# Optimization experiments

Hardware: AMD Instinct MI355X
Metric: run time of the kernel (lower is better)

The kernel has to match this reference:

```python
import jax, jax.numpy as jnp
import numpy as np

GROUPS = 32
EPS = 1e-5
NUM_HEADS = 8
HEAD_DIM = 64
CHANNELS = 512


def group_norm(x, scale, bias):
    # x: [b, h, w, c]; normalize over (h, w, channels-within-group)
    b, h, w, c = x.shape
    xg = x.reshape(b, h, w, GROUPS, c // GROUPS)
    mean = jnp.mean(xg, axis=(1, 2, 4), keepdims=True)
    var = jnp.var(xg, axis=(1, 2, 4), keepdims=True)
    xg = (xg - mean) * jax.lax.rsqrt(var + EPS)
    return xg.reshape(b, h, w, c) * scale + bias


def setup_inputs() -> dict:
    key = jax.random.key(0)
    ks = jax.random.split(key, 8)
    b, hs, ws, c = 8, 32, 32, CHANNELS
    inner = NUM_HEADS * HEAD_DIM
    return {
        "x": jax.random.normal(ks[0], (b, hs, ws, c), dtype=jnp.float32),
        "t": jax.random.normal(ks[1], (b,), dtype=jnp.float32),
        "gn_scale": jnp.ones((c,), dtype=jnp.float32),
        "gn_bias": jnp.zeros((c,), dtype=jnp.float32),
        "w_qkv": jax.random.normal(ks[2], (c, 3 * inner), dtype=jnp.float32) * 0.02,
        "b_qkv": jnp.zeros((3 * inner,), dtype=jnp.float32),
        "w_out": jax.random.normal(ks[3], (inner, c), dtype=jnp.float32) * 0.02,
        "b_out": jnp.zeros((c,), dtype=jnp.float32),
    }


def reference(x, t, gn_scale, gn_bias, w_qkv, b_qkv, w_out, b_out):
    b, hs, ws, c = x.shape
    # NOTE: original reassigns x = GroupNorm(x); the residual uses the NORMALIZED x.
    xn = group_norm(x, gn_scale, gn_bias)
    x_flat = xn.reshape(b, hs * ws, c)                      # [b, s, c]
    qkv = x_flat @ w_qkv + b_qkv                            # [b, s, 3*nh*hd]
    qkv = qkv.reshape(b, hs * ws, NUM_HEADS, 3 * HEAD_DIM)
    q, k, v = jnp.split(qkv, 3, axis=-1)                    # each [b, s, nh, hd]
    q = q / jnp.sqrt(jnp.float32(HEAD_DIM))
    q = q.transpose(0, 2, 1, 3)                             # [b, nh, s, hd]
    k = k.transpose(0, 2, 1, 3)
    v = v.transpose(0, 2, 1, 3)
    attn = jax.nn.softmax(jnp.einsum('bhqd,bhkd->bhqk', q, k), axis=-1)
    out = jnp.einsum('bhqk,bhkd->bhqd', attn, v)            # [b, nh, s, hd]
    out = out.transpose(0, 2, 1, 3).reshape(b, hs * ws, NUM_HEADS * HEAD_DIM)
    h = out @ w_out + b_out                                 # [b, s, c]
    h = h.reshape(b, hs, ws, c)
    return xn + h
```

## Files before the change

### kernel.cpp

```cpp
#include <hip/hip_runtime.h>
#include <hip/hip_bf16.h>


#define B_    8
#define S_    1024
#define C_    512
#define NH    8
#define HD    64
#define QKVC  1536
#define GROUPS 32
#define GSIZE  16
#define EPSV   1e-5f
#define QSCL  0.18033688f

using frag8 = __attribute__((ext_vector_type(8))) short;
using f32x4 = __attribute__((ext_vector_type(4))) float;

__device__ __forceinline__ float bf2f(unsigned short u) {
    union { unsigned int i; float f; } v; v.i = ((unsigned int)u) << 16; return v.f;
}
__device__ __forceinline__ unsigned short f2bf(float f) {
    union { float f; unsigned int i; } v; v.f = f;
    unsigned int x = v.i;
    return (unsigned short)((x + 0x7fffu + ((x >> 16) & 1u)) >> 16);
}
__device__ __forceinline__ unsigned int pk2bf(float a, float b) {
    union { float f; unsigned int u; } x, y; x.f = a; y.f = b;
    return __builtin_amdgcn_perm(y.u + 0x8000u, x.u + 0x8000u, 0x07060302u);
}
__device__ __forceinline__ float fexp2(float x) {
#if __has_builtin(__builtin_amdgcn_exp2f)
    return __builtin_amdgcn_exp2f(x);
#else
    return exp2f(x);
#endif
}
__device__ __forceinline__ f32x4 zero4() {
    f32x4 z; z[0] = 0.f; z[1] = 0.f; z[2] = 0.f; z[3] = 0.f; return z;
}
__device__ __forceinline__ void gl_lds(const unsigned short* gp, unsigned short* lp) {
    __builtin_amdgcn_global_load_lds(
        (const __attribute__((address_space(1))) void*)gp,
        (__attribute__((address_space(3))) void*)lp, 16, 0, 0);
}

__global__ __launch_bounds__(256) void prep_kernel(
        const float* __restrict__ w_qkv, const float* __restrict__ w_out,
        unsigned short* __restrict__ wqkvT, unsigned short* __restrict__ woutT,
        const float* __restrict__ x,
        const float* __restrict__ scale, const float* __restrict__ bias,
        unsigned short* __restrict__ xn) {
    __shared__ float tile[32][33];
    int id = blockIdx.x;
    int t = threadIdx.x;
    if (id < 1024) {
        const float* in; unsigned short* out; int N, n0, k0;
        if (id < 768) { in = w_qkv; out = wqkvT; N = QKVC; n0 = (id % 48) * 32; k0 = (id / 48) * 32; }
        else { int i2 = id - 768; in = w_out; out = woutT; N = C_; n0 = (i2 % 16) * 32; k0 = (i2 / 16) * 32; }
        for (int i = 0; i < 4; ++i) {
            int idx = t + i * 256; int r = idx >> 5, c = idx & 31;
            tile[r][c] = in[(size_t)(k0 + r) * N + n0 + c];
        }
        __syncthreads();
        for (int i = 0; i < 4; ++i) {
            int idx = t + i * 256; int r = idx >> 5, c = idx & 31;
            out[(size_t)(n0 + r) * C_ + k0 + c] = f2bf(tile[c][r]);
        }
        return;
    }
    int bg = id - 1024;
    int b = bg >> 5, g = bg & 31;
    const float* xb = x + (size_t)b * S_ * C_;

    float sum = 0.f, ss = 0.f;
    for (int i = 0; i < 16; ++i) {
        int idx = t + i * 256;
        int row = idx >> 2, j = idx & 3;
        float4 v = *(const float4*)(xb + (size_t)row * C_ + g * GSIZE + j * 4);
        sum += v.x + v.y + v.z + v.w;
        ss  += v.x * v.x + v.y * v.y + v.z * v.z + v.w * v.w;
    }
    for (int off = 1; off < 64; off <<= 1) {
        sum += __shfl_xor(sum, off);
        ss  += __shfl_xor(ss,  off);
    }
    __shared__ float s_sum[4], s_ss[4];
    int wid = t >> 6;
    if ((t & 63) == 0) { s_sum[wid] = sum; s_ss[wid] = ss; }
    __syncthreads();
    sum = s_sum[0] + s_sum[1] + s_sum[2] + s_sum[3];
    ss  = s_ss[0]  + s_ss[1]  + s_ss[2]  + s_ss[3];
    float mean = sum * (1.f / 16384.f);
    float var  = ss * (1.f / 16384.f) - mean * mean;
    float rinv = rsqrtf(var + EPSV);

    float sc[16], bi[16];
    for (int u = 0; u < 16; ++u) {
        sc[u] = scale[g * GSIZE + u];
        bi[u] = bias[g * GSIZE + u];
    }
    for (int i = 0; i < 16; ++i) {
        int idx = t + i * 256;
        int row = idx >> 2, j = idx & 3;
        float4 v = *(const float4*)(xb + (size_t)row * C_ + g * GSIZE + j * 4);
        int c0 = j * 4;
        float f0 = (v.x - mean) * rinv * sc[c0 + 0] + bi[c0 + 0];
        float f1 = (v.y - mean) * rinv * sc[c0 + 1] + bi[c0 + 1];
        float f2 = (v.z - mean) * rinv * sc[c0 + 2] + bi[c0 + 2];
        float f3 = (v.w - mean) * rinv * sc[c0 + 3] + bi[c0 + 3];
        uint2 o;
        o.x = (unsigned int)f2bf(f0) | ((unsigned int)f2bf(f1) << 16);
        o.y = (unsigned int)f2bf(f2) | ((unsigned int)f2bf(f3) << 16);
        *(uint2*)(xn + (size_t)b * S_ * C_ + (size_t)row * C_ + g * GSIZE + c0) = o;
    }
}

template<int MODE>
__global__ __launch_bounds__(256) void gemm_kernel(
        const unsigned short* __restrict__ A,
        const unsigned short* __restrict__ Bt,
        const float* __restrict__ bias,
        const unsigned short* __restrict__ resid,
        unsigned short* __restrict__ outA,
        unsigned short* __restrict__ outV,
        float* __restrict__ outF,
        int M, int N, int K) {
    __shared__ unsigned short As[2][128 * 32];
    __shared__ unsigned short Bs[2][128 * 32];
    int m0 = blockIdx.y * 128, n0 = blockIdx.x * 128;
    int t = threadIdx.x;
    int wid = t >> 6, lane = t & 63;
    int quad = lane >> 4, l16 = lane & 15;
    int wm = (wid >> 1) * 64, wn = (wid & 1) * 64;

    f32x4 acc[4][4];
    for (int mi = 0; mi < 4; ++mi)
        for (int ni = 0; ni < 4; ++ni) acc[mi][ni] = zero4();

    int srow = t >> 2, sseg = t & 3;
    auto stage = [&](int k0, int buf) {
        for (int i = 0; i < 2; ++i) {
            gl_lds(A + (size_t)(m0 + i * 64 + srow) * K + k0 + sseg * 8,
                   &As[buf][(size_t)(i * 256 + wid * 64) * 8]);
            gl_lds(Bt + (size_t)(n0 + i * 64 + srow) * K + k0 + sseg * 8,
                   &Bs[buf][(size_t)(i * 256 + wid * 64) * 8]);
        }
    };

    stage(0, 0);
    int nk = K >> 5;
    for (int i = 0; i < nk; ++i) {
        __syncthreads();
        if (i + 1 < nk) stage((i + 1) << 5, (i + 1) & 1);
        int buf = i & 1;

        frag8 bfrag[4], afrag[4];
        for (int ni = 0; ni < 4; ++ni)
            bfrag[ni] = *(const frag8*)(&Bs[buf][(wn + ni * 16 + l16) * 32 + quad * 8]);
        for (int mi = 0; mi < 4; ++mi)
            afrag[mi] = *(const frag8*)(&As[buf][(wm + mi * 16 + l16) * 32 + quad * 8]);

        for (int mi = 0; mi < 4; ++mi)
            for (int ni = 0; ni < 4; ++ni)
                acc[mi][ni] = __builtin_amdgcn_mfma_f32_16x16x32_bf16(
                    afrag[mi], bfrag[ni], acc[mi][ni], 0, 0, 0);
    }

    for (int ni = 0; ni < 4; ++ni) {
        int c0 = n0 + wn + ni * 16;
        float bv = bias[c0 + l16];
        if (MODE == 0) {
            int h = c0 / 192, rr = c0 % 192;
            if (rr >= 128) {
                int d = rr - 128 + l16;
                int bidx = m0 >> 10;
                unsigned short* vp = outV + (((size_t)bidx * NH + h) * HD + d) * S_
                                   + (m0 & 1023) + wm + quad * 4;
                for (int mi = 0; mi < 4; ++mi) {
                    uint2 pk;
                    pk.x = pk2bf(acc[mi][ni][0] + bv, acc[mi][ni][1] + bv);
                    pk.y = pk2bf(acc[mi][ni][2] + bv, acc[mi][ni][3] + bv);
                    *(uint2*)(vp + mi * 16) = pk;
                }
            } else {
                float scl = (rr < 64) ? QSCL : 1.0f;
                int colk = h * 128 + rr + l16;
                for (int mi = 0; mi < 4; ++mi)
                    for (int r = 0; r < 4; ++r) {
                        int row = m0 + wm + mi * 16 + quad * 4 + r;
                        outA[(size_t)row * 1024 + colk] = f2bf((acc[mi][ni][r] + bv) * scl);
                    }
            }
        } else {
            int col = c0 + l16;
            for (int mi = 0; mi < 4; ++mi)
                for (int r = 0; r < 4; ++r) {
                    int row = m0 + wm + mi * 16 + quad * 4 + r;
                    float v = acc[mi][ni][r] + bv + bf2f(resid[(size_t)row * N + col]);
                    outF[(size_t)row * N + col] = v;
                }
        }
    }
}

__global__ __launch_bounds__(256) void attn_kernel(
        const unsigned short* __restrict__ kq,
        const unsigned short* __restrict__ vT,
        unsigned short* __restrict__ attn_out) {
    int i = blockIdx.x;
    int xcd = i & 7, slot = i >> 3;
    int bh = xcd * 8 + (slot >> 4);
    int qt = slot & 15;
    int b = bh >> 3, h = bh & 7;

    int t = threadIdx.x;
    int wid = t >> 6, lane = t & 63, quad = lane >> 4, l16 = lane & 15;
    int q0 = qt * 64 + wid * 16;

    __shared__ unsigned short Ks[2][2048];
    __shared__ unsigned short Vs[2][2048];

    const unsigned short* qrow = kq + ((size_t)b * S_ + q0 + l16) * 1024 + h * 128;
    frag8 qf0 = *(const frag8*)(qrow + quad * 8);
    frag8 qf1 = *(const frag8*)(qrow + 32 + quad * 8);

    frag8 ones;
    for (int i2 = 0; i2 < 8; ++i2) ones[i2] = (short)0x3f80;

    f32x4 o[4], ol;
    ol = zero4();
    for (int dt = 0; dt < 4; ++dt) o[dt] = zero4();

    const unsigned short* kbase = kq + (size_t)b * S_ * 1024 + h * 128 + 64;
    const unsigned short* vbase = vT + ((size_t)b * NH + h) * HD * S_;

    int kdh = wid & 1, krh = wid >> 1;
    int krow = krh * 16 + (lane >> 2);
    int kseg = lane & 3;
    int vd = wid * 16 + (lane >> 2);
    int vseg = lane & 3;
    int vkh = vseg >> 1, vsp = vseg & 1;
    int vbase1 = vsp * 16 + vkh * 4;

    auto stageK = [&](int j0, int buf) {
        gl_lds(kbase + (size_t)(j0 + krow) * 1024 + kdh * 32 + kseg * 8,
               &Ks[buf][kdh * 1024 + krh * 512]);
    };
    auto loadV = [&](int j0) {
        return *(const uint4*)(vbase + (size_t)vd * S_ + j0 + vseg * 8);
    };
    auto writeV = [&](uint4 w, int buf) {
        unsigned short* vdst = &Vs[buf][vd * 32];
        uint2 g1; g1.x = w.x; g1.y = w.y;
        uint2 g2; g2.x = w.z; g2.y = w.w;
        *(uint2*)(vdst + vbase1)     = g1;
        *(uint2*)(vdst + vbase1 + 8) = g2;
    };

    stageK(0, 0);
    writeV(loadV(0), 0);

    for (int it = 0; it < S_ / 32; ++it) {
        int cur = it & 1, nxt = cur ^ 1;
        __syncthreads();
        uint4 vnext;
        bool more = (it < S_ / 32 - 1);
        if (more) {
            stageK((it + 1) * 32, nxt);
            vnext = loadV((it + 1) * 32);
        }

        frag8 kf[2][2];
        for (int kh = 0; kh < 2; ++kh)
            for (int dh = 0; dh < 2; ++dh)
                kf[kh][dh] = *(const frag8*)(&Ks[cur][dh * 1024 + (kh * 16 + l16) * 32 + quad * 8]);

        f32x4 s[2];
        for (int kh = 0; kh < 2; ++kh) {
            f32x4 acc = zero4();
            acc = __builtin_amdgcn_mfma_f32_16x16x32_bf16(kf[kh][0], qf0, acc, 0, 0, 0);
            acc = __builtin_amdgcn_mfma_f32_16x16x32_bf16(kf[kh][1], qf1, acc, 0, 0, 0);
            s[kh] = acc;
        }

        union { frag8 f; unsigned int u[4]; } pfu;
        pfu.u[0] = pk2bf(fexp2(s[0][0]), fexp2(s[0][1]));
        pfu.u[1] = pk2bf(fexp2(s[0][2]), fexp2(s[0][3]));
        pfu.u[2] = pk2bf(fexp2(s[1][0]), fexp2(s[1][1]));
        pfu.u[3] = pk2bf(fexp2(s[1][2]), fexp2(s[1][3]));

        frag8 vf[4];
        for (int dt = 0; dt < 4; ++dt)
            vf[dt] = *(const frag8*)(&Vs[cur][(dt * 16 + l16) * 32 + quad * 8]);

        ol = __builtin_amdgcn_mfma_f32_16x16x32_bf16(pfu.f, ones, ol, 0, 0, 0);
        for (int dt = 0; dt < 4; ++dt)
            o[dt] = __builtin_amdgcn_mfma_f32_16x16x32_bf16(pfu.f, vf[dt], o[dt], 0, 0, 0);

        if (more) writeV(vnext, nxt);
    }

    for (int r = 0; r < 4; ++r) {
        float inv = 1.0f / ol[r];
        int qrw = q0 + quad * 4 + r;
        for (int dt = 0; dt < 4; ++dt) {
            int ch = h * HD + dt * 16 + l16;
            attn_out[((size_t)b * S_ + qrw) * C_ + ch] = f2bf(o[dt][r] * inv);
        }
    }
}

extern "C" void kernel_launch(void* const* d_in, const int* in_sizes, int n_in,
                              void* d_out, int out_size, void* d_ws, size_t ws_size,
                              hipStream_t stream) {
    const float* x        = (const float*)d_in[0];
    const float* gn_scale = (const float*)d_in[2];
    const float* gn_bias  = (const float*)d_in[3];
    const float* w_qkv    = (const float*)d_in[4];
    const float* b_qkv    = (const float*)d_in[5];
    const float* w_out    = (const float*)d_in[6];
    const float* b_out    = (const float*)d_in[7];
    float* out = (float*)d_out;

    char* ws = (char*)d_ws;
    unsigned short* xn    = (unsigned short*)(ws);
    unsigned short* kq    = (unsigned short*)(ws + ((size_t)8  << 20));
    unsigned short* attn  = (unsigned short*)(ws + ((size_t)24 << 20));
    unsigned short* vT    = (unsigned short*)(ws + ((size_t)32 << 20));
    unsigned short* wqkvT = (unsigned short*)(ws + ((size_t)40 << 20));
    unsigned short* woutT = (unsigned short*)(ws + ((size_t)40 << 20) + ((size_t)3 << 19));

    prep_kernel<<<dim3(1280), 256, 0, stream>>>(
        w_qkv, w_out, wqkvT, woutT, x, gn_scale, gn_bias, xn);

    gemm_kernel<0><<<dim3(QKVC / 128, (B_ * S_) / 128), 256, 0, stream>>>(
        xn, wqkvT, b_qkv, nullptr, kq, vT, nullptr, B_ * S_, QKVC, C_);

    attn_kernel<<<dim3(1024), 256, 0, stream>>>(kq, vT, attn);

    gemm_kernel<1><<<dim3(C_ / 128, (B_ * S_) / 128), 256, 0, stream>>>(
        attn, woutT, b_out, xn, nullptr, nullptr, out, B_ * S_, C_, C_);
}
```

Baseline: 160.2 us.

## Process 64 keys per attention stage and cache GroupNorm input in LDS

The attention kernel now stages two 32-key sub-tiles per pipeline step, which halves the number of barriers and loop iterations and puts more loads in flight, at the cost of doubling K/V shared memory. The GroupNorm branch of the prep kernel stores x as bf16 in shared memory during the statistics pass and reads it back for normalization instead of reading global memory a second time. This adds a bf16 rounding of x before normalization and enlarges the prep kernel's LDS footprint, which may reduce occupancy for the weight-transpose blocks.

```diff
diff --git a/kernel.cpp b/kernel.cpp
--- a/kernel.cpp
+++ b/kernel.cpp
@@ -50,21 +50,23 @@
         const float* __restrict__ x,
         const float* __restrict__ scale, const float* __restrict__ bias,
         unsigned short* __restrict__ xn) {
-    __shared__ float tile[32][33];
+    __shared__ unsigned short xcache[16384];
+    __shared__ float s_red[8];
     int id = blockIdx.x;
     int t = threadIdx.x;
     if (id < 1024) {
+        float* tile = (float*)xcache;
         const float* in; unsigned short* out; int N, n0, k0;
         if (id < 768) { in = w_qkv; out = wqkvT; N = QKVC; n0 = (id % 48) * 32; k0 = (id / 48) * 32; }
         else { int i2 = id - 768; in = w_out; out = woutT; N = C_; n0 = (i2 % 16) * 32; k0 = (i2 / 16) * 32; }
         for (int i = 0; i < 4; ++i) {
             int idx = t + i * 256; int r = idx >> 5, c = idx & 31;
-            tile[r][c] = in[(size_t)(k0 + r) * N + n0 + c];
+            tile[r * 33 + c] = in[(size_t)(k0 + r) * N + n0 + c];
         }
         __syncthreads();
         for (int i = 0; i < 4; ++i) {
             int idx = t + i * 256; int r = idx >> 5, c = idx & 31;
-            out[(size_t)(n0 + r) * C_ + k0 + c] = f2bf(tile[c][r]);
+            out[(size_t)(n0 + r) * C_ + k0 + c] = f2bf(tile[c * 33 + r]);
         }
         return;
     }
@@ -79,17 +81,20 @@
         float4 v = *(const float4*)(xb + (size_t)row * C_ + g * GSIZE + j * 4);
         sum += v.x + v.y + v.z + v.w;
         ss  += v.x * v.x + v.y * v.y + v.z * v.z + v.w * v.w;
+        uint2 c;
+        c.x = pk2bf(v.x, v.y);
+        c.y = pk2bf(v.z, v.w);
+        *(uint2*)(&xcache[idx * 4]) = c;
     }
     for (int off = 1; off < 64; off <<= 1) {
         sum += __shfl_xor(sum, off);
         ss  += __shfl_xor(ss,  off);
     }
-    __shared__ float s_sum[4], s_ss[4];
     int wid = t >> 6;
-    if ((t & 63) == 0) { s_sum[wid] = sum; s_ss[wid] = ss; }
+    if ((t & 63) == 0) { s_red[wid] = sum; s_red[4 + wid] = ss; }
     __syncthreads();
-    sum = s_sum[0] + s_sum[1] + s_sum[2] + s_sum[3];
-    ss  = s_ss[0]  + s_ss[1]  + s_ss[2]  + s_ss[3];
+    sum = s_red[0] + s_red[1] + s_red[2] + s_red[3];
+    ss  = s_red[4] + s_red[5] + s_red[6] + s_red[7];
     float mean = sum * (1.f / 16384.f);
     float var  = ss * (1.f / 16384.f) - mean * mean;
     float rinv = rsqrtf(var + EPSV);
@@ -102,15 +107,19 @@
     for (int i = 0; i < 16; ++i) {
         int idx = t + i * 256;
         int row = idx >> 2, j = idx & 3;
-        float4 v = *(const float4*)(xb + (size_t)row * C_ + g * GSIZE + j * 4);
+        uint2 c = *(const uint2*)(&xcache[idx * 4]);
+        float v0 = bf2f((unsigned short)(c.x & 0xffffu));
+        float v1 = bf2f((unsigned short)(c.x >> 16));
+        float v2 = bf2f((unsigned short)(c.y & 0xffffu));
+        float v3 = bf2f((unsigned short)(c.y >> 16));
         int c0 = j * 4;
-        float f0 = (v.x - mean) * rinv * sc[c0 + 0] + bi[c0 + 0];
-        float f1 = (v.y - mean) * rinv * sc[c0 + 1] + bi[c0 + 1];
-        float f2 = (v.z - mean) * rinv * sc[c0 + 2] + bi[c0 + 2];
-        float f3 = (v.w - mean) * rinv * sc[c0 + 3] + bi[c0 + 3];
+        float f0 = (v0 - mean) * rinv * sc[c0 + 0] + bi[c0 + 0];
+        float f1 = (v1 - mean) * rinv * sc[c0 + 1] + bi[c0 + 1];
+        float f2 = (v2 - mean) * rinv * sc[c0 + 2] + bi[c0 + 2];
+        float f3 = (v3 - mean) * rinv * sc[c0 + 3] + bi[c0 + 3];
         uint2 o;
-        o.x = (unsigned int)f2bf(f0) | ((unsigned int)f2bf(f1) << 16);
-        o.y = (unsigned int)f2bf(f2) | ((unsigned int)f2bf(f3) << 16);
+        o.x = pk2bf(f0, f1);
+        o.y = pk2bf(f2, f3);
         *(uint2*)(xn + (size_t)b * S_ * C_ + (size_t)row * C_ + g * GSIZE + c0) = o;
     }
 }
@@ -217,8 +226,8 @@
     int wid = t >> 6, lane = t & 63, quad = lane >> 4, l16 = lane & 15;
     int q0 = qt * 64 + wid * 16;
 
-    __shared__ unsigned short Ks[2][2048];
-    __shared__ unsigned short Vs[2][2048];
+    __shared__ unsigned short Ks[2][2][2048];
+    __shared__ unsigned short Vs[2][2][2048];
 
     const unsigned short* qrow = kq + ((size_t)b * S_ + q0 + l16) * 1024 + h * 128;
     frag8 qf0 = *(const frag8*)(qrow + quad * 8);
@@ -242,62 +251,70 @@
     int vkh = vseg >> 1, vsp = vseg & 1;
     int vbase1 = vsp * 16 + vkh * 4;
 
-    auto stageK = [&](int j0, int buf) {
+    auto stageK = [&](int j0, int buf, int half) {
         gl_lds(kbase + (size_t)(j0 + krow) * 1024 + kdh * 32 + kseg * 8,
-               &Ks[buf][kdh * 1024 + krh * 512]);
+               &Ks[buf][half][kdh * 1024 + krh * 512]);
     };
     auto loadV = [&](int j0) {
         return *(const uint4*)(vbase + (size_t)vd * S_ + j0 + vseg * 8);
     };
-    auto writeV = [&](uint4 w, int buf) {
-        unsigned short* vdst = &Vs[buf][vd * 32];
+    auto writeV = [&](uint4 w, int buf, int half) {
+        unsigned short* vdst = &Vs[buf][half][vd * 32];
         uint2 g1; g1.x = w.x; g1.y = w.y;
         uint2 g2; g2.x = w.z; g2.y = w.w;
         *(uint2*)(vdst + vbase1)     = g1;
         *(uint2*)(vdst + vbase1 + 8) = g2;
     };
 
-    stageK(0, 0);
-    writeV(loadV(0), 0);
-
-    for (int it = 0; it < S_ / 32; ++it) {
+    stageK(0, 0, 0);  stageK(32, 0, 1);
+    writeV(loadV(0), 0, 0);  writeV(loadV(32), 0, 1);
+
+    for (int it = 0; it < S_ / 64; ++it) {
         int cur = it & 1, nxt = cur ^ 1;
         __syncthreads();
-        uint4 vnext;
-        bool more = (it < S_ / 32 - 1);
+        uint4 vn0, vn1;
+        bool more = (it < S_ / 64 - 1);
         if (more) {
-            stageK((it + 1) * 32, nxt);
-            vnext = loadV((it + 1) * 32);
-        }
-
-        frag8 kf[2][2];
-        for (int kh = 0; kh < 2; ++kh)
-            for (int dh = 0; dh < 2; ++dh)
-                kf[kh][dh] = *(const frag8*)(&Ks[cur][dh * 1024 + (kh * 16 + l16) * 32 + quad * 8]);
-
-        f32x4 s[2];
-        for (int kh = 0; kh < 2; ++kh) {
-            f32x4 acc = zero4();
-            acc = __builtin_amdgcn_mfma_f32_16x16x32_bf16(kf[kh][0], qf0, acc, 0, 0, 0);
-            acc = __builtin_amdgcn_mfma_f32_16x16x32_bf16(kf[kh][1], qf1, acc, 0, 0, 0);
-            s[kh] = acc;
-        }
-
-        union { frag8 f; unsigned int u[4]; } pfu;
-        pfu.u[0] = pk2bf(fexp2(s[0][0]), fexp2(s[0][1]));
-        pfu.u[1] = pk2bf(fexp2(s[0][2]), fexp2(s[0][3]));
-        pfu.u[2] = pk2bf(fexp2(s[1][0]), fexp2(s[1][1]));
-        pfu.u[3] = pk2bf(fexp2(s[1][2]), fexp2(s[1][3]));
-
-        frag8 vf[4];
-        for (int dt = 0; dt < 4; ++dt)
-            vf[dt] = *(const frag8*)(&Vs[cur][(dt * 16 + l16) * 32 + quad * 8]);
-
-        ol = __builtin_amdgcn_mfma_f32_16x16x32_bf16(pfu.f, ones, ol, 0, 0, 0);
-        for (int dt = 0; dt < 4; ++dt)
-            o[dt] = __builtin_amdgcn_mfma_f32_16x16x32_bf16(pfu.f, vf[dt], o[dt], 0, 0, 0);
-
-        if (more) writeV(vnext, nxt);
+            int jn = (it + 1) * 64;
+            stageK(jn, nxt, 0);
+            stageK(jn + 32, nxt, 1);
+            vn0 = loadV(jn);
+            vn1 = loadV(jn + 32);
+        }
+
+        for (int half = 0; half < 2; ++half) {
+            frag8 kf[2][2];
+            for (int kh = 0; kh < 2; ++kh)
+                for (int dh = 0; dh < 2; ++dh)
+                    kf[kh][dh] = *(const frag8*)(&Ks[cur][half][dh * 1024 + (kh * 16 + l16) * 32 + quad * 8]);
+
+            f32x4 s[2];
+            for (int kh = 0; kh < 2; ++kh) {
+                f32x4 acc = zero4();
+                acc = __builtin_amdgcn_mfma_f32_16x16x32_bf16(kf[kh][0], qf0, acc, 0, 0, 0);
+                acc = __builtin_amdgcn_mfma_f32_16x16x32_bf16(kf[kh][1], qf1, acc, 0, 0, 0);
+                s[kh] = acc;
+            }
+
+            union { frag8 f; unsigned int u[4]; } pfu;
+            pfu.u[0] = pk2bf(fexp2(s[0][0]), fexp2(s[0][1]));
+            pfu.u[1] = pk2bf(fexp2(s[0][2]), fexp2(s[0][3]));
+            pfu.u[2] = pk2bf(fexp2(s[1][0]), fexp2(s[1][1]));
+            pfu.u[3] = pk2bf(fexp2(s[1][2]), fexp2(s[1][3]));
+
+            frag8 vf[4];
+            for (int dt = 0; dt < 4; ++dt)
+                vf[dt] = *(const frag8*)(&Vs[cur][half][(dt * 16 + l16) * 32 + quad * 8]);
+
+            ol = __builtin_amdgcn_mfma_f32_16x16x32_bf16(pfu.f, ones, ol, 0, 0, 0);
+            for (int dt = 0; dt < 4; ++dt)
+                o[dt] = __builtin_amdgcn_mfma_f32_16x16x32_bf16(pfu.f, vf[dt], o[dt], 0, 0, 0);
+        }
+
+        if (more) {
+            writeV(vn0, nxt, 0);
+            writeV(vn1, nxt, 1);
+        }
     }
 
     for (int r = 0; r < 4; ++r) {
```

Result: no change. 157.2 us (-1.9%).
